# Optimization experiments

Measured on AMD Instinct MI355X. Metric: run time of the kernel, lower is better.

Reference implementation:

```python
import jax, jax.numpy as jnp
import numpy as np

D_MODEL = 1024
NUM_HEADS = 16
HEAD_DIM = D_MODEL // NUM_HEADS


def setup_inputs() -> dict:
    key = jax.random.key(0)
    ks = jax.random.split(key, 11)
    N, S = 4, 2048
    s = 1.0 / np.sqrt(D_MODEL)
    return {
        "query": jax.random.normal(ks[0], (N, S, D_MODEL), jnp.float32),
        "key": jax.random.normal(ks[1], (N, S, D_MODEL), jnp.float32),
        "value": jax.random.normal(ks[2], (N, S, D_MODEL), jnp.float32),
        "Wq": jax.random.normal(ks[3], (D_MODEL, D_MODEL), jnp.float32) * s,
        "bq": jnp.zeros((D_MODEL,), jnp.float32),
        "Wk": jax.random.normal(ks[4], (D_MODEL, D_MODEL), jnp.float32) * s,
        "bk": jnp.zeros((D_MODEL,), jnp.float32),
        "Wv": jax.random.normal(ks[5], (D_MODEL, D_MODEL), jnp.float32) * s,
        "bv": jnp.zeros((D_MODEL,), jnp.float32),
        "Wo": jax.random.normal(ks[6], (D_MODEL, D_MODEL), jnp.float32) * s,
        "bo": jnp.zeros((D_MODEL,), jnp.float32),
    }


def reference(query, key, value, Wq, bq, Wk, bk, Wv, bv, Wo, bo):
    N, Q, _ = query.shape
    K = key.shape[1]
    # torch Linear: x @ W^T + b
    q = (query @ Wq.T + bq).reshape(N, Q, NUM_HEADS, HEAD_DIM)
    k = (key @ Wk.T + bk).reshape(N, K, NUM_HEADS, HEAD_DIM)
    v = (value @ Wv.T + bv).reshape(N, K, NUM_HEADS, HEAD_DIM)
    # NOTE: original module applies NO 1/sqrt(head_dim) scaling.
    scores = jnp.einsum('nqhd,nkhd->nhqk', q, k)
    attn = jax.nn.softmax(scores, axis=3)
    out = jnp.einsum('nhqk,nkhd->nqhd', attn, v).reshape(N, Q, D_MODEL)
    return out @ Wo.T + bo
```

## Files before the change

### kernel.cpp

```cpp
#include <hip/hip_runtime.h>
#include <stdint.h>

#define SEQ 2048
#define MROWS 8192
#define LOG2E 1.44269504f

typedef __attribute__((ext_vector_type(8))) _Float16 f16x8;
typedef __attribute__((ext_vector_type(2))) __fp16 fp16x2_t;
typedef __attribute__((ext_vector_type(8))) unsigned short ushort8;
typedef __attribute__((ext_vector_type(4))) unsigned short ushort4_t;
typedef __attribute__((ext_vector_type(4))) float f32x4;

__device__ __forceinline__ unsigned short f32_to_f16u(float f) {
  union { _Float16 h; unsigned short u; } v; v.h = (_Float16)f; return v.u;
}

__global__ __launch_bounds__(256) void qkv_k(
    const float* __restrict__ Aq, const float* __restrict__ Ak, const float* __restrict__ Av,
    const float* __restrict__ Wq, const float* __restrict__ Wk, const float* __restrict__ Wv,
    const float* __restrict__ bq, const float* __restrict__ bk, const float* __restrict__ bv,
    unsigned short* __restrict__ Qf, unsigned short* __restrict__ Kf, unsigned short* __restrict__ Vt)
{
  const int z = blockIdx.z;
  const float* __restrict__ A    = (z==0)? Aq : (z==1)? Ak : Av;
  const float* __restrict__ W    = (z==0)? Wq : (z==1)? Wk : Wv;
  const float* __restrict__ bias = (z==0)? bq : (z==1)? bk : bv;

  __shared__ unsigned short Ah[128*32];
  __shared__ unsigned short Bh[128*32];

  const int tid  = threadIdx.x;
  const int lane = tid & 63;
  const int w    = tid >> 6;
  const int wm   = w >> 1, wn = w & 1;
  const int row0 = blockIdx.x * 128;
  const int col0 = blockIdx.y * 128;

  f32x4 acc[4][4] = {};

  for (int k0 = 0; k0 < 1024; k0 += 32) {
    __syncthreads();
    #pragma unroll
    for (int i = 0; i < 2; ++i) {
      int c = tid + i*256;
      int r = c >> 2, slot = c & 3;
      int lidx = r*32 + ((slot ^ ((r >> 1) & 3))*8);
      {
        const float* ap = A + (size_t)(row0 + r)*1024 + k0 + slot*8;
        float4 f0 = *(const float4*)ap;
        float4 f1 = *(const float4*)(ap + 4);
        float fs[8] = {f0.x,f0.y,f0.z,f0.w,f1.x,f1.y,f1.z,f1.w};
        ushort8 hv;
        #pragma unroll
        for (int j=0;j<8;++j) hv[j] = f32_to_f16u(fs[j]);
        *(ushort8*)&Ah[lidx] = hv;
      }
      {
        const float* bp = W + (size_t)(col0 + r)*1024 + k0 + slot*8;
        float4 f0 = *(const float4*)bp;
        float4 f1 = *(const float4*)(bp + 4);
        float fs[8] = {f0.x,f0.y,f0.z,f0.w,f1.x,f1.y,f1.z,f1.w};
        ushort8 hv;
        #pragma unroll
        for (int j=0;j<8;++j) hv[j] = f32_to_f16u(fs[j]);
        *(ushort8*)&Bh[lidx] = hv;
      }
    }
    __syncthreads();

    f16x8 a_[4], b_[4];
    const int slotR = lane >> 4;
    #pragma unroll
    for (int m=0;m<4;++m) {
      int r = wm*64 + m*16 + (lane & 15);
      a_[m] = *(const f16x8*)&Ah[r*32 + ((slotR ^ ((r>>1)&3))*8)];
    }
    #pragma unroll
    for (int nn=0;nn<4;++nn) {
      int r = wn*64 + nn*16 + (lane & 15);
      b_[nn] = *(const f16x8*)&Bh[r*32 + ((slotR ^ ((r>>1)&3))*8)];
    }
    #pragma unroll
    for (int m=0;m<4;++m)
      #pragma unroll
      for (int nn=0;nn<4;++nn)
        acc[m][nn] = __builtin_amdgcn_mfma_f32_16x16x32_f16(a_[m], b_[nn], acc[m][nn],0,0,0);
  }

  #pragma unroll
  for (int m=0;m<4;++m) {
    #pragma unroll
    for (int nn=0;nn<4;++nn) {
      int gcol = col0 + wn*64 + nn*16 + (lane & 15);
      float bsv = bias[gcol];
      if (z == 2) {
        int rbase = row0 + wm*64 + m*16 + (lane>>4)*4;
        int nIdx = rbase >> 11, s0 = rbase & 2047;
        ushort4_t pk;
        #pragma unroll
        for (int r2=0;r2<4;++r2) pk[r2] = f32_to_f16u(acc[m][nn][r2] + bsv);
        *(ushort4_t*)&Vt[((size_t)(nIdx*1024 + gcol))*2048 + s0] = pk;
      } else {
        unsigned short* __restrict__ dst = (z==0)? Qf : Kf;
        const float qsc = (z==0)? LOG2E : 1.0f;
        #pragma unroll
        for (int r2=0;r2<4;++r2) {
          int grow = row0 + wm*64 + m*16 + (lane>>4)*4 + r2;
          dst[(size_t)grow*1024 + gcol] = f32_to_f16u((acc[m][nn][r2] + bsv) * qsc);
        }
      }
    }
  }
}

__global__ __launch_bounds__(256) void oproj_k(
    const unsigned short* __restrict__ AO, const float* __restrict__ W,
    const float* __restrict__ bias, float* __restrict__ out)
{
  __shared__ unsigned short Ah[128*32];
  __shared__ unsigned short Bh[128*32];

  const int tid  = threadIdx.x;
  const int lane = tid & 63;
  const int w    = tid >> 6;
  const int wm   = w >> 1, wn = w & 1;
  const int row0 = blockIdx.x * 128;
  const int col0 = blockIdx.y * 128;

  f32x4 acc[4][4] = {};

  for (int k0 = 0; k0 < 1024; k0 += 32) {
    __syncthreads();
    #pragma unroll
    for (int i = 0; i < 2; ++i) {
      int c = tid + i*256;
      int r = c >> 2, slot = c & 3;
      int lidx = r*32 + ((slot ^ ((r >> 1) & 3))*8);
      *(ushort8*)&Ah[lidx] = *(const ushort8*)&AO[(size_t)(row0 + r)*1024 + k0 + slot*8];
      {
        const float* bp = W + (size_t)(col0 + r)*1024 + k0 + slot*8;
        float4 f0 = *(const float4*)bp;
        float4 f1 = *(const float4*)(bp + 4);
        float fs[8] = {f0.x,f0.y,f0.z,f0.w,f1.x,f1.y,f1.z,f1.w};
        ushort8 hv;
        #pragma unroll
        for (int j=0;j<8;++j) hv[j] = f32_to_f16u(fs[j]);
        *(ushort8*)&Bh[lidx] = hv;
      }
    }
    __syncthreads();

    f16x8 a_[4], b_[4];
    const int slotR = lane >> 4;
    #pragma unroll
    for (int m=0;m<4;++m) {
      int r = wm*64 + m*16 + (lane & 15);
      a_[m] = *(const f16x8*)&Ah[r*32 + ((slotR ^ ((r>>1)&3))*8)];
    }
    #pragma unroll
    for (int nn=0;nn<4;++nn) {
      int r = wn*64 + nn*16 + (lane & 15);
      b_[nn] = *(const f16x8*)&Bh[r*32 + ((slotR ^ ((r>>1)&3))*8)];
    }
    #pragma unroll
    for (int m=0;m<4;++m)
      #pragma unroll
      for (int nn=0;nn<4;++nn)
        acc[m][nn] = __builtin_amdgcn_mfma_f32_16x16x32_f16(a_[m], b_[nn], acc[m][nn],0,0,0);
  }

  #pragma unroll
  for (int m=0;m<4;++m)
    #pragma unroll
    for (int nn=0;nn<4;++nn) {
      int gcol = col0 + wn*64 + nn*16 + (lane & 15);
      float bsv = bias[gcol];
      #pragma unroll
      for (int r2=0;r2<4;++r2) {
        int grow = row0 + wm*64 + m*16 + (lane>>4)*4 + r2;
        out[(size_t)grow*1024 + gcol] = acc[m][nn][r2] + bsv;
      }
    }
}

__global__ __launch_bounds__(256) void attn_k(
  const unsigned short* __restrict__ Qf, const unsigned short* __restrict__ Kf,
  const unsigned short* __restrict__ Vt, unsigned short* __restrict__ AO)
{
  __shared__ unsigned short Ks[2][64*64];
  __shared__ unsigned short Vs[2][64*64];
  __shared__ unsigned short Ps[4][16*64];

  const int tid = threadIdx.x, lane = tid & 63, w = tid >> 6;
  const int q = lane & 15, g = lane >> 4;

  const int bid = blockIdx.x;
  const int swz = (bid & 7) * 128 + (bid >> 3);
  const int qt = swz & 15, nh = swz >> 4;
  const int n = nh >> 4, h = nh & 15;

  f16x8 qf[2][2];
  #pragma unroll
  for (int qm=0; qm<2; ++qm) {
    int qrow = n*SEQ + qt*128 + w*32 + qm*16 + q;
    #pragma unroll
    for (int ks=0; ks<2; ++ks)
      qf[qm][ks] = *(const f16x8*)&Qf[(size_t)qrow*1024 + h*64 + ks*32 + g*8];
  }

  f32x4 o[2][4] = {};
  float mrun[2] = {-1e30f,-1e30f}, lrun[2] = {0.f,0.f};

  const size_t kbase = (size_t)(n*SEQ)*1024 + h*64;
  const size_t vbase = ((size_t)(n*1024 + h*64))*SEQ;

  #pragma unroll
  for (int i=0;i<2;++i){
    int c = tid + i*256; int r = c>>3, sl = c&7;
    int lidx = r*64 + ((sl^(r&7))*8);
    *(ushort8*)&Ks[0][lidx] = *(const ushort8*)&Kf[kbase + (size_t)r*1024 + sl*8];
    *(ushort8*)&Vs[0][lidx] = *(const ushort8*)&Vt[vbase + (size_t)r*SEQ + sl*8];
  }
  __syncthreads();

  int cur = 0;
  for (int kt = 0; kt < 32; ++kt) {
    f32x4 s[2][4];
    #pragma unroll
    for (int qm=0;qm<2;++qm)
      #pragma unroll
      for (int nf=0; nf<4; ++nf) s[qm][nf] = f32x4{0.f,0.f,0.f,0.f};
    __builtin_amdgcn_s_setprio(1);
    #pragma unroll
    for (int nf=0; nf<4; ++nf) {
      int rr = nf*16 + q;
      #pragma unroll
      for (int ks=0; ks<2; ++ks) {
        f16x8 kb = *(const f16x8*)&Ks[cur][rr*64 + (((ks*4+g)^(q&7))*8)];
        s[0][nf] = __builtin_amdgcn_mfma_f32_16x16x32_f16(kb, qf[0][ks], s[0][nf],0,0,0);
        s[1][nf] = __builtin_amdgcn_mfma_f32_16x16x32_f16(kb, qf[1][ks], s[1][nf],0,0,0);
      }
    }
    __builtin_amdgcn_s_setprio(0);

    ushort8 kreg[2], vreg[2];
    if (kt < 31) {
      #pragma unroll
      for (int i=0;i<2;++i){
        int c = tid + i*256; int r = c>>3, sl = c&7;
        kreg[i] = *(const ushort8*)&Kf[kbase + (size_t)((kt+1)*64 + r)*1024 + sl*8];
        vreg[i] = *(const ushort8*)&Vt[vbase + (size_t)r*SEQ + (kt+1)*64 + sl*8];
      }
    }

    #pragma unroll
    for (int qm=0; qm<2; ++qm) {
      float ml = fmaxf(fmaxf(fmaxf(s[qm][0][0],s[qm][0][1]),fmaxf(s[qm][0][2],s[qm][0][3])),
                       fmaxf(fmaxf(s[qm][1][0],s[qm][1][1]),fmaxf(s[qm][1][2],s[qm][1][3])));
      float mh = fmaxf(fmaxf(fmaxf(s[qm][2][0],s[qm][2][1]),fmaxf(s[qm][2][2],s[qm][2][3])),
                       fmaxf(fmaxf(s[qm][3][0],s[qm][3][1]),fmaxf(s[qm][3][2],s[qm][3][3])));
      ml = fmaxf(ml, mh);
      if (!__all(ml <= mrun[qm] + 7.0f)) {
        float m1 = fmaxf(ml, __shfl_xor(ml, 16, 64));
        float m2 = fmaxf(m1, __shfl_xor(m1, 32, 64));
        float mn = fmaxf(mrun[qm], m2);
        float sc = __builtin_amdgcn_exp2f(mrun[qm] - mn);
        lrun[qm] *= sc;
        mrun[qm] = mn;
        #pragma unroll
        for (int df=0; df<4; ++df)
          #pragma unroll
          for (int r=0;r<4;++r) o[qm][df][r] *= sc;
      }
      float m0 = mrun[qm];
      float pvv[16]; float rsl = 0.f;
      #pragma unroll
      for (int nf=0; nf<4; ++nf)
        #pragma unroll
        for (int r=0;r<4;++r) {
          float p = __builtin_amdgcn_exp2f(s[qm][nf][r] - m0);
          pvv[nf*4+r] = p; rsl += p;
        }
      float rsc = rsl;
      rsc += __shfl_xor(rsc, 16, 64);
      rsc += __shfl_xor(rsc, 32, 64);
      lrun[qm] += rsc;

      #pragma unroll
      for (int nf=0; nf<4; ++nf) {
        union { fp16x2_t h2[2]; ushort4_t u4; } pk;
        pk.h2[0] = __builtin_amdgcn_cvt_pkrtz(pvv[nf*4+0], pvv[nf*4+1]);
        pk.h2[1] = __builtin_amdgcn_cvt_pkrtz(pvv[nf*4+2], pvv[nf*4+3]);
        int gi = 2*nf + (g>>1);
        int idx = q*64 + ((gi ^ (q&7))*8) + (g&1)*4;
        *(ushort4_t*)&Ps[w][idx] = pk.u4;
      }

      #pragma unroll
      for (int s2=0; s2<2; ++s2) {
        int sl = 4*s2 + g;
        f16x8 pa = *(const f16x8*)&Ps[w][q*64 + ((sl^(q&7))*8)];
        __builtin_amdgcn_s_setprio(1);
        #pragma unroll
        for (int df=0; df<4; ++df) {
          f16x8 vb = *(const f16x8*)&Vs[cur][(df*16+q)*64 + ((sl^(q&7))*8)];
          o[qm][df] = __builtin_amdgcn_mfma_f32_16x16x32_f16(vb, pa, o[qm][df],0,0,0);
        }
        __builtin_amdgcn_s_setprio(0);
      }
    }

    if (kt < 31) {
      #pragma unroll
      for (int i=0;i<2;++i){
        int c = tid + i*256; int r = c>>3, sl = c&7;
        int lidx = r*64 + ((sl^(r&7))*8);
        *(ushort8*)&Ks[cur^1][lidx] = kreg[i];
        *(ushort8*)&Vs[cur^1][lidx] = vreg[i];
      }
    }
    __syncthreads();
    cur ^= 1;
  }

  #pragma unroll
  for (int qm=0; qm<2; ++qm) {
    float inv = 1.0f / lrun[qm];
    int qrow = n*SEQ + qt*128 + w*32 + qm*16 + q;
    #pragma unroll
    for (int df=0; df<4; ++df)
      #pragma unroll
      for (int r=0;r<4;++r)
        AO[(size_t)qrow*1024 + h*64 + df*16 + g*4 + r] = f32_to_f16u(o[qm][df][r] * inv);
  }
}

extern "C" void kernel_launch(void* const* d_in, const int* in_sizes, int n_in,
                              void* d_out, int out_size, void* d_ws, size_t ws_size,
                              hipStream_t stream)
{
  (void)in_sizes; (void)n_in; (void)out_size; (void)ws_size;
  const float* query = (const float*)d_in[0];
  const float* key   = (const float*)d_in[1];
  const float* value = (const float*)d_in[2];
  const float* Wq = (const float*)d_in[3];
  const float* bq = (const float*)d_in[4];
  const float* Wk = (const float*)d_in[5];
  const float* bk = (const float*)d_in[6];
  const float* Wv = (const float*)d_in[7];
  const float* bv = (const float*)d_in[8];
  const float* Wo = (const float*)d_in[9];
  const float* bo = (const float*)d_in[10];
  float* out = (float*)d_out;

  unsigned short* ws = (unsigned short*)d_ws;
  const size_t PLANE = (size_t)MROWS * 1024;
  unsigned short* Qf = ws;
  unsigned short* Kf = Qf + PLANE;
  unsigned short* Vt = Kf + PLANE;
  unsigned short* AO = Vt + PLANE;

  dim3 bb(256);
  qkv_k <<<dim3(64,8,3), bb, 0, stream>>>(query,key,value, Wq,Wk,Wv, bq,bk,bv, Qf,Kf,Vt);
  attn_k<<<dim3(1024), bb, 0, stream>>>(Qf, Kf, Vt, AO);
  oproj_k<<<dim3(64,8), bb, 0, stream>>>(AO, Wo, bo, out);
}
```

Measured before the change: 251.4 us.

## Pre-convert weights to fp16, load GEMM tiles via global_load_lds, batch PV MFMAs

Adds a kernel that converts all four weight matrices to fp16 once per call, so the projection GEMMs load half the weight bytes and skip per-tile conversion. Weight tiles, and the AO tiles in the output projection, are copied straight into LDS with global_load_lds instead of going through registers. Activations are packed with cvt_pkrtz instead of per-element conversion. In attention, both query sub-tiles' P values are staged before the PV MFMAs, which are interleaved, and the cross-lane row-sum reduction is deferred to the end. The trade-offs are an extra launch plus workspace, and round-toward-zero rounding of the inputs.

Measured after the change: 221.6 us. 11.9% less time.

```diff
diff --git a/kernel.cpp b/kernel.cpp
--- a/kernel.cpp
+++ b/kernel.cpp
@@ -15,15 +15,43 @@
   union { _Float16 h; unsigned short u; } v; v.h = (_Float16)f; return v.u;
 }
 
+__device__ __forceinline__ ushort8 pack8_rtz(float4 f0, float4 f1) {
+  union { fp16x2_t h2[4]; ushort8 u8; } pk;
+  pk.h2[0] = __builtin_amdgcn_cvt_pkrtz(f0.x, f0.y);
+  pk.h2[1] = __builtin_amdgcn_cvt_pkrtz(f0.z, f0.w);
+  pk.h2[2] = __builtin_amdgcn_cvt_pkrtz(f1.x, f1.y);
+  pk.h2[3] = __builtin_amdgcn_cvt_pkrtz(f1.z, f1.w);
+  return pk.u8;
+}
+
+__device__ __forceinline__ void gload16(const void* g, void* l) {
+  __builtin_amdgcn_global_load_lds(
+      (const __attribute__((address_space(1))) unsigned int*)g,
+      (__attribute__((address_space(3))) unsigned int*)l, 16, 0, 0);
+}
+
+__global__ __launch_bounds__(256) void wconv_k(
+    const float* __restrict__ Wq, const float* __restrict__ Wk,
+    const float* __restrict__ Wv, const float* __restrict__ Wo,
+    unsigned short* __restrict__ WF)
+{
+  const int plane = blockIdx.y;
+  const float* __restrict__ s = (plane==0)? Wq : (plane==1)? Wk : (plane==2)? Wv : Wo;
+  size_t off = ((size_t)blockIdx.x*256 + threadIdx.x) * 8;
+  float4 f0 = *(const float4*)(s + off);
+  float4 f1 = *(const float4*)(s + off + 4);
+  *(ushort8*)&WF[(size_t)plane*1048576 + off] = pack8_rtz(f0, f1);
+}
+
 __global__ __launch_bounds__(256) void qkv_k(
     const float* __restrict__ Aq, const float* __restrict__ Ak, const float* __restrict__ Av,
-    const float* __restrict__ Wq, const float* __restrict__ Wk, const float* __restrict__ Wv,
+    const unsigned short* __restrict__ WF,
     const float* __restrict__ bq, const float* __restrict__ bk, const float* __restrict__ bv,
     unsigned short* __restrict__ Qf, unsigned short* __restrict__ Kf, unsigned short* __restrict__ Vt)
 {
   const int z = blockIdx.z;
   const float* __restrict__ A    = (z==0)? Aq : (z==1)? Ak : Av;
-  const float* __restrict__ W    = (z==0)? Wq : (z==1)? Wk : Wv;
+  const unsigned short* __restrict__ W = WF + (size_t)z*1048576;
   const float* __restrict__ bias = (z==0)? bq : (z==1)? bk : bv;
 
   __shared__ unsigned short Ah[128*32];
@@ -41,30 +69,20 @@
   for (int k0 = 0; k0 < 1024; k0 += 32) {
     __syncthreads();
     #pragma unroll
+    for (int j=0;j<2;++j) {
+      int r  = w*32 + j*16 + (lane>>2);
+      int sl = (lane & 3) ^ ((r>>1)&3);
+      gload16(W + (size_t)(col0 + r)*1024 + k0 + sl*8, &Bh[(w*32 + j*16)*32]);
+    }
+    #pragma unroll
     for (int i = 0; i < 2; ++i) {
       int c = tid + i*256;
       int r = c >> 2, slot = c & 3;
       int lidx = r*32 + ((slot ^ ((r >> 1) & 3))*8);
-      {
-        const float* ap = A + (size_t)(row0 + r)*1024 + k0 + slot*8;
-        float4 f0 = *(const float4*)ap;
-        float4 f1 = *(const float4*)(ap + 4);
-        float fs[8] = {f0.x,f0.y,f0.z,f0.w,f1.x,f1.y,f1.z,f1.w};
-        ushort8 hv;
-        #pragma unroll
-        for (int j=0;j<8;++j) hv[j] = f32_to_f16u(fs[j]);
-        *(ushort8*)&Ah[lidx] = hv;
-      }
-      {
-        const float* bp = W + (size_t)(col0 + r)*1024 + k0 + slot*8;
-        float4 f0 = *(const float4*)bp;
-        float4 f1 = *(const float4*)(bp + 4);
-        float fs[8] = {f0.x,f0.y,f0.z,f0.w,f1.x,f1.y,f1.z,f1.w};
-        ushort8 hv;
-        #pragma unroll
-        for (int j=0;j<8;++j) hv[j] = f32_to_f16u(fs[j]);
-        *(ushort8*)&Bh[lidx] = hv;
-      }
+      const float* ap = A + (size_t)(row0 + r)*1024 + k0 + slot*8;
+      float4 f0 = *(const float4*)ap;
+      float4 f1 = *(const float4*)(ap + 4);
+      *(ushort8*)&Ah[lidx] = pack8_rtz(f0, f1);
     }
     __syncthreads();
 
@@ -114,7 +132,7 @@
 }
 
 __global__ __launch_bounds__(256) void oproj_k(
-    const unsigned short* __restrict__ AO, const float* __restrict__ W,
+    const unsigned short* __restrict__ AO, const unsigned short* __restrict__ W,
     const float* __restrict__ bias, float* __restrict__ out)
 {
   __shared__ unsigned short Ah[128*32];
@@ -132,21 +150,11 @@
   for (int k0 = 0; k0 < 1024; k0 += 32) {
     __syncthreads();
     #pragma unroll
-    for (int i = 0; i < 2; ++i) {
-      int c = tid + i*256;
-      int r = c >> 2, slot = c & 3;
-      int lidx = r*32 + ((slot ^ ((r >> 1) & 3))*8);
-      *(ushort8*)&Ah[lidx] = *(const ushort8*)&AO[(size_t)(row0 + r)*1024 + k0 + slot*8];
-      {
-        const float* bp = W + (size_t)(col0 + r)*1024 + k0 + slot*8;
-        float4 f0 = *(const float4*)bp;
-        float4 f1 = *(const float4*)(bp + 4);
-        float fs[8] = {f0.x,f0.y,f0.z,f0.w,f1.x,f1.y,f1.z,f1.w};
-        ushort8 hv;
-        #pragma unroll
-        for (int j=0;j<8;++j) hv[j] = f32_to_f16u(fs[j]);
-        *(ushort8*)&Bh[lidx] = hv;
-      }
+    for (int j=0;j<2;++j) {
+      int r  = w*32 + j*16 + (lane>>2);
+      int sl = (lane & 3) ^ ((r>>1)&3);
+      gload16(AO + (size_t)(row0 + r)*1024 + k0 + sl*8, &Ah[(w*32 + j*16)*32]);
+      gload16(W  + (size_t)(col0 + r)*1024 + k0 + sl*8, &Bh[(w*32 + j*16)*32]);
     }
     __syncthreads();
 
@@ -189,7 +197,7 @@
 {
   __shared__ unsigned short Ks[2][64*64];
   __shared__ unsigned short Vs[2][64*64];
-  __shared__ unsigned short Ps[4][16*64];
+  __shared__ unsigned short Ps[4][32*64];
 
   const int tid = threadIdx.x, lane = tid & 63, w = tid >> 6;
   const int q = lane & 15, g = lane >> 4;
@@ -281,10 +289,7 @@
           float p = __builtin_amdgcn_exp2f(s[qm][nf][r] - m0);
           pvv[nf*4+r] = p; rsl += p;
         }
-      float rsc = rsl;
-      rsc += __shfl_xor(rsc, 16, 64);
-      rsc += __shfl_xor(rsc, 32, 64);
-      lrun[qm] += rsc;
+      lrun[qm] += rsl;
 
       #pragma unroll
       for (int nf=0; nf<4; ++nf) {
@@ -292,22 +297,24 @@
         pk.h2[0] = __builtin_amdgcn_cvt_pkrtz(pvv[nf*4+0], pvv[nf*4+1]);
         pk.h2[1] = __builtin_amdgcn_cvt_pkrtz(pvv[nf*4+2], pvv[nf*4+3]);
         int gi = 2*nf + (g>>1);
-        int idx = q*64 + ((gi ^ (q&7))*8) + (g&1)*4;
+        int idx = (qm*16+q)*64 + ((gi ^ (q&7))*8) + (g&1)*4;
         *(ushort4_t*)&Ps[w][idx] = pk.u4;
       }
-
-      #pragma unroll
-      for (int s2=0; s2<2; ++s2) {
-        int sl = 4*s2 + g;
-        f16x8 pa = *(const f16x8*)&Ps[w][q*64 + ((sl^(q&7))*8)];
-        __builtin_amdgcn_s_setprio(1);
-        #pragma unroll
-        for (int df=0; df<4; ++df) {
-          f16x8 vb = *(const f16x8*)&Vs[cur][(df*16+q)*64 + ((sl^(q&7))*8)];
-          o[qm][df] = __builtin_amdgcn_mfma_f32_16x16x32_f16(vb, pa, o[qm][df],0,0,0);
-        }
-        __builtin_amdgcn_s_setprio(0);
-      }
+    }
+
+    #pragma unroll
+    for (int s2=0; s2<2; ++s2) {
+      int sl = 4*s2 + g;
+      f16x8 pa0 = *(const f16x8*)&Ps[w][(q    )*64 + ((sl^(q&7))*8)];
+      f16x8 pa1 = *(const f16x8*)&Ps[w][(16+q)*64 + ((sl^(q&7))*8)];
+      __builtin_amdgcn_s_setprio(1);
+      #pragma unroll
+      for (int df=0; df<4; ++df) {
+        f16x8 vb = *(const f16x8*)&Vs[cur][(df*16+q)*64 + ((sl^(q&7))*8)];
+        o[0][df] = __builtin_amdgcn_mfma_f32_16x16x32_f16(vb, pa0, o[0][df],0,0,0);
+        o[1][df] = __builtin_amdgcn_mfma_f32_16x16x32_f16(vb, pa1, o[1][df],0,0,0);
+      }
+      __builtin_amdgcn_s_setprio(0);
     }
 
     if (kt < 31) {
@@ -325,7 +332,10 @@
 
   #pragma unroll
   for (int qm=0; qm<2; ++qm) {
-    float inv = 1.0f / lrun[qm];
+    float rs = lrun[qm];
+    rs += __shfl_xor(rs, 16, 64);
+    rs += __shfl_xor(rs, 32, 64);
+    float inv = 1.0f / rs;
     int qrow = n*SEQ + qt*128 + w*32 + qm*16 + q;
     #pragma unroll
     for (int df=0; df<4; ++df)
@@ -359,9 +369,11 @@
   unsigned short* Kf = Qf + PLANE;
   unsigned short* Vt = Kf + PLANE;
   unsigned short* AO = Vt + PLANE;
+  unsigned short* WF = AO + PLANE;
 
   dim3 bb(256);
-  qkv_k <<<dim3(64,8,3), bb, 0, stream>>>(query,key,value, Wq,Wk,Wv, bq,bk,bv, Qf,Kf,Vt);
+  wconv_k<<<dim3(512,4), bb, 0, stream>>>(Wq, Wk, Wv, Wo, WF);
+  qkv_k <<<dim3(64,8,3), bb, 0, stream>>>(query,key,value, WF, bq,bk,bv, Qf,Kf,Vt);
   attn_k<<<dim3(1024), bb, 0, stream>>>(Qf, Kf, Vt, AO);
-  oproj_k<<<dim3(64,8), bb, 0, stream>>>(AO, Wo, bo, out);
-}
+  oproj_k<<<dim3(64,8), bb, 0, stream>>>(AO, WF + 3*1048576, bo, out);
+}
```
